# Kernel optimization log

Measured on AMD Instinct MI355X. Metric: run time of the kernel, lower is better.

The kernel has to match this reference:

```python
import jax, jax.numpy as jnp
import numpy as np

D = 192      # model dim (out_channels)
DIN = 384    # d_inner = 2*D
N = 16       # d_state
DTR = 12     # dt_rank = ceil(D/16)
K = 4        # depthwise conv kernel size
NB = 3       # total mamba blocks (2 stacked + 1 in downsample)


def setup_inputs() -> dict:
    key = jax.random.key(0)
    ks = jax.random.split(key, 8)
    rn = lambda k, shape, s: jax.random.normal(k, shape, jnp.float32) * s
    inp = {
        "x": jax.random.normal(ks[0], (2, 96, 56, 56), jnp.float32),
        "proj_w": rn(ks[1], (D, 96), 0.1),
        "proj_b": jnp.zeros((D,), jnp.float32),
        "bn_g": jnp.ones((D,), jnp.float32),
        "bn_b": jnp.zeros((D,), jnp.float32),
        "bn_mean": jnp.zeros((D,), jnp.float32),
        "bn_var": jnp.ones((D,), jnp.float32),
        "ln_g": jnp.ones((NB, D), jnp.float32),
        "ln_b": jnp.zeros((NB, D), jnp.float32),
        "Win": rn(ks[2], (NB, 2 * DIN, D), 0.05),
        "b_in": jnp.zeros((NB, 2 * DIN), jnp.float32),
        "conv_w": rn(ks[3], (NB, DIN, K), 0.2),
        "conv_b": jnp.zeros((NB, DIN), jnp.float32),
        "Wx": rn(ks[4], (NB, DTR + 2 * N, DIN), 0.05),
        "Wdt": rn(ks[5], (NB, DIN, DTR), 0.05),
        "bdt": jnp.full((NB, DIN), -4.6, jnp.float32),  # softplus ~ 0.01
        "A_log": jnp.log(jnp.broadcast_to(jnp.arange(1, N + 1, dtype=jnp.float32), (NB, DIN, N))),
        "Dskip": jnp.ones((NB, DIN), jnp.float32),
        "Wout": rn(ks[6], (NB, D, DIN), 0.05),
        "bout": jnp.zeros((NB, D), jnp.float32),
    }
    return inp


def _mamba(x, ln_g, ln_b, Win, b_in, conv_w, conv_b, Wx, Wdt, bdt, A_log, Dskip, Wout, bout):
    # x: (B, C, H, W) -> flatten spatial dims to a sequence (B, L, C)
    B, C, H, W = x.shape
    L = H * W
    seq = x.reshape(B, C, L).transpose(0, 2, 1)
    mu = seq.mean(-1, keepdims=True)
    var = seq.var(-1, keepdims=True)
    h = (seq - mu) * jax.lax.rsqrt(var + 1e-5) * ln_g + ln_b  # LayerNorm
    xz = jnp.einsum('bld,ed->ble', h, Win) + b_in              # (B, L, 2*DIN)
    xi, z = jnp.split(xz, 2, axis=-1)
    # depthwise causal conv1d along L
    xc = jnp.pad(xi.transpose(0, 2, 1), ((0, 0), (0, 0), (K - 1, 0)))
    xc = jax.lax.conv_general_dilated(xc, conv_w[:, None, :], (1,), 'VALID',
                                      feature_group_count=DIN) + conv_b[:, None]
    xi = jax.nn.silu(xc).transpose(0, 2, 1)                    # (B, L, DIN)
    proj = jnp.einsum('ble,pe->blp', xi, Wx)                   # (B, L, DTR+2N)
    dtl = proj[..., :DTR]
    Bm = proj[..., DTR:DTR + N]
    Cm = proj[..., DTR + N:]
    dt = jax.nn.softplus(jnp.einsum('blr,er->ble', dtl, Wdt) + bdt)  # (B, L, DIN)
    A = -jnp.exp(A_log)                                         # (DIN, N)
    dA = jnp.exp(dt[..., None] * A)                             # (B, L, DIN, N)
    dBx = (dt * xi)[..., None] * Bm[:, :, None, :]              # (B, L, DIN, N)

    def step(hc, t):
        dA_t, dBx_t, C_t = t
        hc = dA_t * hc + dBx_t                                  # (B, DIN, N)
        return hc, jnp.einsum('ben,bn->be', hc, C_t)

    h0 = jnp.zeros((B, DIN, N), x.dtype)
    _, ys = jax.lax.scan(step, h0, (dA.transpose(1, 0, 2, 3),
                                    dBx.transpose(1, 0, 2, 3),
                                    Cm.transpose(1, 0, 2)))
    y = ys.transpose(1, 0, 2) + Dskip * xi
    y = y * jax.nn.silu(z)
    out = jnp.einsum('ble,de->bld', y, Wout) + bout
    return out.transpose(0, 2, 1).reshape(B, C, H, W)


def _maxpool2(x):
    return jax.lax.reduce_window(x, -jnp.inf, jax.lax.max,
                                 (1, 1, 2, 2), (1, 1, 2, 2), 'VALID')


def reference(x, proj_w, proj_b, bn_g, bn_b, bn_mean, bn_var, ln_g, ln_b, Win, b_in,
              conv_w, conv_b, Wx, Wdt, bdt, A_log, Dskip, Wout, bout):
    # proj (conv1x1) + BatchNorm (eval-mode running stats)
    x = jnp.einsum('bchw,oc->bohw', x, proj_w) + proj_b[:, None, None]
    x = (x - bn_mean[:, None, None]) * jax.lax.rsqrt(bn_var[:, None, None] + 1e-5) \
        * bn_g[:, None, None] + bn_b[:, None, None]
    blk = lambda i, v: _mamba(v, ln_g[i], ln_b[i], Win[i], b_in[i], conv_w[i], conv_b[i],
                              Wx[i], Wdt[i], bdt[i], A_log[i], Dskip[i], Wout[i], bout[i])
    for i in range(2):  # residual mamba blocks
        x = x + blk(i, x)
    skip = x
    x = blk(2, _maxpool2(x))  # downsample: maxpool then mamba (no residual)
    return (x, skip)
```

## Files before the change

kernel.cpp:

```cpp
#include <hip/hip_runtime.h>

typedef __attribute__((ext_vector_type(8))) __bf16 bf16x8;
typedef __attribute__((ext_vector_type(4))) __bf16 bf16x4;
typedef __attribute__((ext_vector_type(4))) float f32x4;

#define DEV static __device__ __forceinline__

DEV float fast_rcp(float x) { return __builtin_amdgcn_rcpf(x); }
DEV float sigm(float x) { return fast_rcp(1.f + __expf(-x)); }
DEV float siluf(float x) { return x * sigm(x); }
DEV float softplusf(float x) { return x > 20.f ? x : __logf(1.f + __expf(x)); }

__global__ __launch_bounds__(256) void k_wcvt(
    const float* __restrict__ Win, const float* __restrict__ Wout,
    const float* __restrict__ Wx, __bf16* __restrict__ Wb)
{
  const int idx = blockIdx.x * 256 + threadIdx.x;
  if (idx < 442368) Wb[idx] = (__bf16)Win[idx];
  else if (idx < 663552) Wb[idx] = (__bf16)Wout[idx - 442368];
  else if (idx < 714240) Wb[idx] = (__bf16)Wx[idx - 663552];
}

__global__ __launch_bounds__(256) void k_proj(
    const float* __restrict__ x, const float* __restrict__ pw,
    const float* __restrict__ pb, const float* __restrict__ bng,
    const float* __restrict__ bnb, const float* __restrict__ bnm,
    const float* __restrict__ bnv, float* __restrict__ v)
{
  constexpr int SAP = 104;
  __shared__ __bf16 As[64 * SAP];
  __shared__ __bf16 Ws[64 * SAP];
  const int tid = threadIdx.x;
  const int r0 = blockIdx.x * 64;
  const int col0 = blockIdx.y * 64;
  const int b = r0 / 3136, l0 = r0 % 3136;
  const int lane = tid & 63, wv = tid >> 6;
  const int rh = wv >> 1, ch = wv & 1;
  const int lm = lane & 15, quad = lane >> 4;

#pragma unroll
  for (int it = 0; it < 6; ++it) {
    const int idx = tid + it * 256;
    const int c = idx >> 4, l4 = idx & 15;
    const float4 t = *(const float4*)(x + ((size_t)(b * 96 + c)) * 3136 + l0 + l4 * 4);
    As[(l4 * 4 + 0) * SAP + c] = (__bf16)t.x;
    As[(l4 * 4 + 1) * SAP + c] = (__bf16)t.y;
    As[(l4 * 4 + 2) * SAP + c] = (__bf16)t.z;
    As[(l4 * 4 + 3) * SAP + c] = (__bf16)t.w;
  }
#pragma unroll
  for (int it = 0; it < 6; ++it) {
    const int idx = tid + it * 256;
    const int wr = idx / 24, kc = (idx % 24) * 4;
    const float4 t = *(const float4*)(pw + (size_t)(col0 + wr) * 96 + kc);
    bf16x4 o;
    o[0] = (__bf16)t.x; o[1] = (__bf16)t.y; o[2] = (__bf16)t.z; o[3] = (__bf16)t.w;
    *(bf16x4*)(&Ws[wr * SAP + kc]) = o;
  }
  __syncthreads();

  f32x4 acc[2][2] = {};
#pragma unroll
  for (int ks = 0; ks < 3; ++ks) {
    const int kb = ks * 32 + quad * 8;
    bf16x8 a0 = *(const bf16x8*)(&As[(rh * 32 + lm) * SAP + kb]);
    bf16x8 a1 = *(const bf16x8*)(&As[(rh * 32 + 16 + lm) * SAP + kb]);
    bf16x8 b0 = *(const bf16x8*)(&Ws[(ch * 32 + lm) * SAP + kb]);
    bf16x8 b1 = *(const bf16x8*)(&Ws[(ch * 32 + 16 + lm) * SAP + kb]);
    acc[0][0] = __builtin_amdgcn_mfma_f32_16x16x32_bf16(a0, b0, acc[0][0], 0, 0, 0);
    acc[0][1] = __builtin_amdgcn_mfma_f32_16x16x32_bf16(a0, b1, acc[0][1], 0, 0, 0);
    acc[1][0] = __builtin_amdgcn_mfma_f32_16x16x32_bf16(a1, b0, acc[1][0], 0, 0, 0);
    acc[1][1] = __builtin_amdgcn_mfma_f32_16x16x32_bf16(a1, b1, acc[1][1], 0, 0, 0);
  }

#pragma unroll
  for (int ti = 0; ti < 2; ++ti)
#pragma unroll
    for (int tj = 0; tj < 2; ++tj) {
      const int gcol = col0 + ch * 32 + tj * 16 + lm;
      const float s = rsqrtf(bnv[gcol] + 1e-5f) * bng[gcol];
      const float sh = (pb[gcol] - bnm[gcol]) * s + bnb[gcol];
#pragma unroll
      for (int j = 0; j < 4; ++j) {
        const int grow = r0 + rh * 32 + ti * 16 + quad * 4 + j;
        v[(size_t)grow * 192 + gcol] = acc[ti][tj][j] * s + sh;
      }
    }
}

__global__ __launch_bounds__(256) void k_pool(const float* __restrict__ v, float* __restrict__ vp)
{
  const int idx = blockIdx.x * 256 + threadIdx.x;
  if (idx >= 1568 * 192) return;
  const int d = idx % 192;
  const int r2 = idx / 192;
  const int b = r2 / 784, l2 = r2 % 784;
  const int h2 = l2 / 28, w2 = l2 % 28;
  const float* p = v + (size_t)(b * 3136 + h2 * 112 + w2 * 2) * 192 + d;
  vp[idx] = fmaxf(fmaxf(p[0], p[192]), fmaxf(p[56 * 192], p[57 * 192]));
}

__global__ __launch_bounds__(256) void k_conv(
    const float* __restrict__ xz, float* __restrict__ xi, __bf16* __restrict__ xiB,
    const float* __restrict__ cw, const float* __restrict__ cb,
    int Lseq, int nthreads)
{
  const int idx = blockIdx.x * 256 + threadIdx.x;
  if (idx >= nthreads) return;
  const int e = idx % 384;
  const int seg = idx / 384;
  const int nseg = Lseq / 8;
  const int b = seg / nseg;
  const int l0 = (seg % nseg) * 8;
  const float4 w4 = *(const float4*)(cw + e * 4);
  const float bv = cb[e];
  float xv[11];
#pragma unroll
  for (int k = 0; k < 11; ++k) {
    const int l = l0 - 3 + k;
    xv[k] = (l >= 0) ? xz[(size_t)(b * Lseq + l) * 768 + e] : 0.f;
  }
#pragma unroll
  for (int j = 0; j < 8; ++j) {
    const float a = bv + xv[j] * w4.x + xv[j + 1] * w4.y + xv[j + 2] * w4.z + xv[j + 3] * w4.w;
    const float r = siluf(a);
    const size_t o = (size_t)(b * Lseq + l0 + j) * 384 + e;
    xi[o] = r;
    xiB[o] = (__bf16)r;
  }
}

constexpr int EPI_XZ = 0, EPI_G2 = 1, EPI_RES = 2, EPI_RES_SKIP = 3, EPI_OUT2 = 4;

template <int AMODE, int NT, int EPI>
__global__ __launch_bounds__(256) void k_gemm(
    const void* __restrict__ Ain, const __bf16* __restrict__ W,
    const float* __restrict__ bias, float* __restrict__ O,
    int M, int K, int Nvalid,
    float* __restrict__ dtlbuf, float* __restrict__ bcbuf,
    float* __restrict__ oflt,
    const float* __restrict__ lng, const float* __restrict__ lnb,
    int Lseq)
{
  constexpr int SA = 200;
  constexpr int CT = (NT == 1) ? 2 : 4;
  __shared__ __bf16 As[64 * SA];
  __shared__ __bf16 Ws[64 * NT * SA];
  __shared__ float lnS[(AMODE == 2) ? 384 : 1];
  const int tid = threadIdx.x;
  const int r0 = blockIdx.x * 64;
  const int col0 = blockIdx.y * (64 * NT);
  const int lane = tid & 63, wv = tid >> 6;
  const int rh = (NT == 1) ? (wv >> 1) : (wv & 1);
  const int ch = (NT == 1) ? (wv & 1) : (wv >> 1);
  const int lm = lane & 15, quad = lane >> 4;

  if constexpr (AMODE == 2) {
    if (tid < 192) { lnS[tid] = lng[tid]; lnS[192 + tid] = lnb[tid]; }
    __syncthreads();
  }

  f32x4 acc[2][CT] = {};
  const int nkp = K / 192;
  for (int kp = 0; kp < nkp; ++kp) {
    if (kp) __syncthreads();
    if constexpr (AMODE == 1) {
      const __bf16* Ab = (const __bf16*)Ain;
#pragma unroll
      for (int it = 0; it < 6; ++it) {
        const int idx = tid + it * 256;
        const int row = idx / 24, kc = (idx % 24) * 8;
        const int gr = min(r0 + row, M - 1);
        bf16x8 val = *(const bf16x8*)(Ab + (size_t)gr * K + kp * 192 + kc);
        *(bf16x8*)(&As[row * SA + kc]) = val;
      }
    } else {
      const float* A = (const float*)Ain;
      const int row = tid >> 2, part = tid & 3;
      const int gr = min(r0 + row, M - 1);
      const int cbase = part * 48;
      float4 tv[12];
#pragma unroll
      for (int j = 0; j < 12; ++j)
        tv[j] = *(const float4*)(A + (size_t)gr * 192 + cbase + j * 4);
      float s = 0.f, sq = 0.f;
#pragma unroll
      for (int j = 0; j < 12; ++j) {
        s += tv[j].x + tv[j].y + tv[j].z + tv[j].w;
        sq += tv[j].x * tv[j].x + tv[j].y * tv[j].y + tv[j].z * tv[j].z + tv[j].w * tv[j].w;
      }
      s += __shfl_xor(s, 1); s += __shfl_xor(s, 2);
      sq += __shfl_xor(sq, 1); sq += __shfl_xor(sq, 2);
      const float mean = s * (1.f / 192.f);
      const float rstd = rsqrtf(sq * (1.f / 192.f) - mean * mean + 1e-5f);
#pragma unroll
      for (int j = 0; j < 12; ++j) {
        const int c = cbase + j * 4;
        bf16x4 o;
        o[0] = (__bf16)((tv[j].x - mean) * rstd * lnS[c + 0] + lnS[192 + c + 0]);
        o[1] = (__bf16)((tv[j].y - mean) * rstd * lnS[c + 1] + lnS[192 + c + 1]);
        o[2] = (__bf16)((tv[j].z - mean) * rstd * lnS[c + 2] + lnS[192 + c + 2]);
        o[3] = (__bf16)((tv[j].w - mean) * rstd * lnS[c + 3] + lnS[192 + c + 3]);
        *(bf16x4*)(&As[row * SA + c]) = o;
      }
    }
#pragma unroll
    for (int it = 0; it < 6 * NT; ++it) {
      const int idx = tid + it * 256;
      const int wr = idx / 24, kc = (idx % 24) * 8;
      const int gw = col0 + wr;
      bf16x8 val = {};
      if (gw < Nvalid) val = *(const bf16x8*)(W + (size_t)gw * K + kp * 192 + kc);
      *(bf16x8*)(&Ws[wr * SA + kc]) = val;
    }
    __syncthreads();
#pragma unroll
    for (int ks = 0; ks < 6; ++ks) {
      const int kb = ks * 32 + quad * 8;
      bf16x8 a0 = *(const bf16x8*)(&As[(rh * 32 + lm) * SA + kb]);
      bf16x8 a1 = *(const bf16x8*)(&As[(rh * 32 + 16 + lm) * SA + kb]);
#pragma unroll
      for (int tj = 0; tj < CT; ++tj) {
        bf16x8 bfr = *(const bf16x8*)(&Ws[(ch * (16 * CT) + tj * 16 + lm) * SA + kb]);
        acc[0][tj] = __builtin_amdgcn_mfma_f32_16x16x32_bf16(a0, bfr, acc[0][tj], 0, 0, 0);
        acc[1][tj] = __builtin_amdgcn_mfma_f32_16x16x32_bf16(a1, bfr, acc[1][tj], 0, 0, 0);
      }
    }
  }

  if constexpr (EPI == EPI_G2) {
    __shared__ float dtlS[64 * 12];
#pragma unroll
    for (int ti = 0; ti < 2; ++ti)
#pragma unroll
      for (int tj = 0; tj < CT; ++tj) {
        const int colt = ch * (16 * CT) + tj * 16 + lm;
#pragma unroll
        for (int j = 0; j < 4; ++j) {
          const int rowt = rh * 32 + ti * 16 + quad * 4 + j;
          const int grow = r0 + rowt;
          const float val = acc[ti][tj][j];
          if (colt < 12) dtlS[rowt * 12 + colt] = val;
          else if (colt < 44 && grow < M)
            bcbuf[(size_t)grow * 32 + (colt - 12)] = val;
        }
      }
    __syncthreads();
    for (int idx = tid; idx < 64 * 12; idx += 256) {
      const int grow = r0 + idx / 12;
      if (grow < M) dtlbuf[(size_t)grow * 12 + idx % 12] = dtlS[idx];
    }
  } else {
#pragma unroll
    for (int ti = 0; ti < 2; ++ti)
#pragma unroll
      for (int tj = 0; tj < CT; ++tj) {
        const int colt = ch * (16 * CT) + tj * 16 + lm;
        const int gcol = col0 + colt;
        const float bv = bias[gcol];
#pragma unroll
        for (int j = 0; j < 4; ++j) {
          const int rowt = rh * 32 + ti * 16 + quad * 4 + j;
          const int grow = r0 + rowt;
          if (grow >= M) continue;
          const float val = acc[ti][tj][j] + bv;
          if constexpr (EPI == EPI_XZ) {
            O[(size_t)grow * 768 + gcol] = val;
          } else if constexpr (EPI == EPI_RES) {
            O[(size_t)grow * 192 + gcol] += val;
          } else if constexpr (EPI == EPI_RES_SKIP) {
            const float nv = O[(size_t)grow * 192 + gcol] + val;
            O[(size_t)grow * 192 + gcol] = nv;
            const int b = grow / 3136, l = grow % 3136;
            oflt[b * 602112 + gcol * 3136 + l] = nv;
          } else {
            const int b = grow / 784, l = grow % 784;
            oflt[b * 150528 + gcol * 784 + l] = val;
          }
        }
      }
  }
}

constexpr int SC_LC = 28, SC_T = 7, SC_TN = 4;

DEV void compute_dts(const float* __restrict__ dtl, const float* __restrict__ Wdt,
                     const float* __restrict__ bdt, int rowbase, int e, int t,
                     float* dtlS, float* wdtS, float* dts)
{
  for (int idx = t; idx < SC_LC * 12; idx += 128)
    dtlS[idx] = dtl[(size_t)(rowbase + idx / 12) * 12 + idx % 12];
#pragma unroll
  for (int r = 0; r < 12; ++r) wdtS[r * 128 + t] = Wdt[(size_t)e * 12 + r];
}

__global__ __launch_bounds__(128) void k_scan1(
    const float* __restrict__ dtl, const float* __restrict__ xi,
    const float* __restrict__ bc, const float* __restrict__ Wdt,
    const float* __restrict__ bdt, const float* __restrict__ A_log,
    float* __restrict__ P, float* __restrict__ S, int Lseq, int NC)
{
  __shared__ float Bs[SC_LC * 16];
  __shared__ float dts[SC_LC * 128];
  __shared__ float dtlS[SC_LC * 12];
  __shared__ float wdtS[12 * 128];
  const int t = threadIdx.x;
  const int e = blockIdx.y * 128 + t;
  const int c = blockIdx.x % NC;
  const int b = blockIdx.x / NC;
  const int rowbase = b * Lseq + c * SC_LC;

  for (int idx = t; idx < SC_LC * 16; idx += 128) {
    const int l = idx >> 4, q = idx & 15;
    Bs[idx] = bc[(size_t)(rowbase + l) * 32 + q];
  }
  compute_dts(dtl, Wdt, bdt, rowbase, e, t, dtlS, wdtS, dts);
  const float bdte = bdt[e];

  float An2[16];
  {
    const float4* a4 = (const float4*)(A_log + e * 16);
    float4 t0 = a4[0], t1 = a4[1], t2 = a4[2], t3 = a4[3];
    float tmp[16] = {t0.x, t0.y, t0.z, t0.w, t1.x, t1.y, t1.z, t1.w,
                     t2.x, t2.y, t2.z, t2.w, t3.x, t3.y, t3.z, t3.w};
#pragma unroll
    for (int n = 0; n < 16; ++n) An2[n] = -__expf(tmp[n]) * 1.44269504f;
  }
  __syncthreads();
  for (int l = 0; l < SC_LC; ++l) {
    float a = bdte;
#pragma unroll
    for (int r = 0; r < 12; ++r) a += dtlS[l * 12 + r] * wdtS[r * 128 + t];
    dts[l * 128 + t] = softplusf(a);
  }

  float h[16], ap[16];
#pragma unroll
  for (int n = 0; n < 16; ++n) { h[n] = 0.f; ap[n] = 1.f; }

  float xA[SC_T], xB[SC_T];
  auto LOADA = [&](int tt) {
#pragma unroll
    for (int j = 0; j < SC_T; ++j)
      xA[j] = xi[(size_t)(rowbase + tt * SC_T + j) * 384 + e];
  };
  auto LOADB = [&](int tt) {
#pragma unroll
    for (int j = 0; j < SC_T; ++j)
      xB[j] = xi[(size_t)(rowbase + tt * SC_T + j) * 384 + e];
  };
  auto COMP = [&](const float (&x8)[SC_T], int tt) {
#pragma unroll
    for (int j = 0; j < SC_T; ++j) {
      const int l = tt * SC_T + j;
      const float dtv = dts[l * 128 + t];
      const float u = dtv * x8[j];
      const float* Brow = &Bs[l * 16];
#pragma unroll
      for (int n = 0; n < 16; ++n) {
        const float a = __builtin_amdgcn_exp2f(dtv * An2[n]);
        h[n] = a * h[n] + u * Brow[n];
        ap[n] *= a;
      }
    }
  };

  LOADA(0);
#pragma unroll
  for (int tt = 0; tt < SC_TN; ++tt) {
    if (tt & 1) { if (tt + 1 < SC_TN) LOADA(tt + 1); COMP(xB, tt); }
    else        { if (tt + 1 < SC_TN) LOADB(tt + 1); COMP(xA, tt); }
  }

  const size_t o = ((size_t)(b * NC + c) * 384 + e) * 16;
#pragma unroll
  for (int q = 0; q < 4; ++q) {
    *(float4*)(P + o + q * 4) = make_float4(ap[q*4], ap[q*4+1], ap[q*4+2], ap[q*4+3]);
    *(float4*)(S + o + q * 4) = make_float4(h[q*4], h[q*4+1], h[q*4+2], h[q*4+3]);
  }
}

__global__ __launch_bounds__(256) void k_carry(
    const float* __restrict__ P, float* __restrict__ SH, int NC)
{
  const int tid = blockIdx.x * 256 + threadIdx.x;
  const int b = tid / 6144, r = tid % 6144;
  size_t o = (size_t)b * NC * 6144 + r;
  float h = 0.f;
  for (int c0 = 0; c0 < NC; c0 += 4) {
    float p[4], s[4];
#pragma unroll
    for (int k = 0; k < 4; ++k) { p[k] = P[o + (size_t)k * 6144]; s[k] = SH[o + (size_t)k * 6144]; }
#pragma unroll
    for (int k = 0; k < 4; ++k) { SH[o + (size_t)k * 6144] = h; h = p[k] * h + s[k]; }
    o += (size_t)4 * 6144;
  }
}

__global__ __launch_bounds__(128) void k_scan2(
    const float* __restrict__ dtl, const float* __restrict__ xi,
    const float* __restrict__ bc, const float* __restrict__ xz,
    const float* __restrict__ Wdt, const float* __restrict__ bdt,
    const float* __restrict__ A_log, const float* __restrict__ Dskip,
    const float* __restrict__ H0, __bf16* __restrict__ y, int Lseq, int NC)
{
  __shared__ float BCs[SC_LC * 32];
  __shared__ float dts[SC_LC * 128];
  __shared__ float dtlS[SC_LC * 12];
  __shared__ float wdtS[12 * 128];
  const int t = threadIdx.x;
  const int e = blockIdx.y * 128 + t;
  const int c = blockIdx.x % NC;
  const int b = blockIdx.x / NC;
  const int rowbase = b * Lseq + c * SC_LC;

  for (int idx = t; idx < SC_LC * 32; idx += 128)
    BCs[idx] = bc[(size_t)rowbase * 32 + idx];
  compute_dts(dtl, Wdt, bdt, rowbase, e, t, dtlS, wdtS, dts);
  const float bdte = bdt[e];

  float An2[16];
  {
    const float4* a4 = (const float4*)(A_log + e * 16);
    float4 t0 = a4[0], t1 = a4[1], t2 = a4[2], t3 = a4[3];
    float tmp[16] = {t0.x, t0.y, t0.z, t0.w, t1.x, t1.y, t1.z, t1.w,
                     t2.x, t2.y, t2.z, t2.w, t3.x, t3.y, t3.z, t3.w};
#pragma unroll
    for (int n = 0; n < 16; ++n) An2[n] = -__expf(tmp[n]) * 1.44269504f;
  }
  float h[16];
  {
    const size_t o = ((size_t)(b * NC + c) * 384 + e) * 16;
    const float4* h4 = (const float4*)(H0 + o);
    float4 t0 = h4[0], t1 = h4[1], t2 = h4[2], t3 = h4[3];
    h[0]=t0.x; h[1]=t0.y; h[2]=t0.z; h[3]=t0.w;
    h[4]=t1.x; h[5]=t1.y; h[6]=t1.z; h[7]=t1.w;
    h[8]=t2.x; h[9]=t2.y; h[10]=t2.z; h[11]=t2.w;
    h[12]=t3.x; h[13]=t3.y; h[14]=t3.z; h[15]=t3.w;
  }
  __syncthreads();
  for (int l = 0; l < SC_LC; ++l) {
    float a = bdte;
#pragma unroll
    for (int r = 0; r < 12; ++r) a += dtlS[l * 12 + r] * wdtS[r * 128 + t];
    dts[l * 128 + t] = softplusf(a);
  }
  const float Dse = Dskip[e];

  float xA[SC_T], zA[SC_T], xB[SC_T], zB[SC_T];
  auto LOADA = [&](int tt) {
#pragma unroll
    for (int j = 0; j < SC_T; ++j) {
      const size_t r = (size_t)(rowbase + tt * SC_T + j);
      xA[j] = xi[r * 384 + e];
      zA[j] = xz[r * 768 + 384 + e];
    }
  };
  auto LOADB = [&](int tt) {
#pragma unroll
    for (int j = 0; j < SC_T; ++j) {
      const size_t r = (size_t)(rowbase + tt * SC_T + j);
      xB[j] = xi[r * 384 + e];
      zB[j] = xz[r * 768 + 384 + e];
    }
  };
  auto COMP = [&](const float (&x8)[SC_T], const float (&z8)[SC_T], int tt) {
#pragma unroll
    for (int j = 0; j < SC_T; ++j) {
      const int l = tt * SC_T + j;
      const float dtv = dts[l * 128 + t];
      const float xiv = x8[j];
      const float u = dtv * xiv;
      const float* Brow = &BCs[l * 32];
      const float* Crow = Brow + 16;
      float yv = 0.f;
#pragma unroll
      for (int n = 0; n < 16; ++n) {
        const float a = __builtin_amdgcn_exp2f(dtv * An2[n]);
        h[n] = a * h[n] + u * Brow[n];
        yv += h[n] * Crow[n];
      }
      y[(size_t)(rowbase + l) * 384 + e] = (__bf16)((yv + Dse * xiv) * siluf(z8[j]));
    }
  };

  LOADA(0);
#pragma unroll
  for (int tt = 0; tt < SC_TN; ++tt) {
    if (tt & 1) { if (tt + 1 < SC_TN) LOADA(tt + 1); COMP(xB, zB, tt); }
    else        { if (tt + 1 < SC_TN) LOADB(tt + 1); COMP(xA, zA, tt); }
  }
}

extern "C" void kernel_launch(void* const* d_in, const int* in_sizes, int n_in,
                              void* d_out, int out_size, void* d_ws, size_t ws_size,
                              hipStream_t stream)
{
  const float* x    = (const float*)d_in[0];
  const float* pw   = (const float*)d_in[1];
  const float* pb   = (const float*)d_in[2];
  const float* bng  = (const float*)d_in[3];
  const float* bnb  = (const float*)d_in[4];
  const float* bnm  = (const float*)d_in[5];
  const float* bnv  = (const float*)d_in[6];
  const float* lng  = (const float*)d_in[7];
  const float* lnb  = (const float*)d_in[8];
  const float* Win  = (const float*)d_in[9];
  const float* b_in = (const float*)d_in[10];
  const float* cw   = (const float*)d_in[11];
  const float* cb   = (const float*)d_in[12];
  const float* Wx   = (const float*)d_in[13];
  const float* Wdt  = (const float*)d_in[14];
  const float* bdt  = (const float*)d_in[15];
  const float* Alog = (const float*)d_in[16];
  const float* Dsk  = (const float*)d_in[17];
  const float* Wout = (const float*)d_in[18];
  const float* bout = (const float*)d_in[19];

  float* wsf = (float*)d_ws;
  float* v    = wsf;
  float* xz   = v + 1204224;
  float* xib  = xz + 4816896;
  float* dtlb = xib + 2408448;
  float* bcb  = dtlb + 75264;
  float* Sb   = bcb + 200704;
  float* vp   = Sb + 1376256;
  __bf16* xiB = (__bf16*)(vp + 301056);
  __bf16* yB  = xiB;
  __bf16* Wb  = (__bf16*)(vp + 301056 + 1204224);

  float* out0 = (float*)d_out;
  float* out1 = out0 + 301056;
  float* Pbig = out0;
  float* Psml = xz + 2408448;

  k_wcvt<<<2790, 256, 0, stream>>>(Win, Wout, Wx, Wb);
  k_proj<<<dim3(98, 3), 256, 0, stream>>>(x, pw, pb, bng, bnb, bnm, bnv, v);

  for (int i = 0; i < 3; ++i) {
    const int big = (i < 2) ? 1 : 0;
    const int Lseq = big ? 3136 : 784;
    const int M = 2 * Lseq;
    const int NC = Lseq / SC_LC;
    const int MB = (M + 63) / 64;
    const float* lng_i = lng + i * 192;
    const float* lnb_i = lnb + i * 192;
    const float* bin_i = b_in + i * 768;
    const float* cw_i  = cw + i * 384 * 4;
    const float* cb_i  = cb + i * 384;
    const float* Wdt_i = Wdt + i * 384 * 12;
    const float* bdt_i = bdt + i * 384;
    const float* Al_i  = Alog + i * 384 * 16;
    const float* Ds_i  = Dsk + i * 384;
    const float* bo_i  = bout + i * 192;
    const __bf16* Winb_i  = Wb + i * 147456;
    const __bf16* Woutb_i = Wb + 442368 + i * 73728;
    const __bf16* Wxb_i   = Wb + 663552 + i * 16896;
    float* Pb = big ? Pbig : Psml;

    if (i == 2)
      k_pool<<<(1568 * 192 + 255) / 256, 256, 0, stream>>>(v, vp);
    const float* src = big ? v : vp;

    k_gemm<2, 2, EPI_XZ><<<dim3(MB, 6), 256, 0, stream>>>(
        src, Winb_i, bin_i, xz, M, 192, 768,
        nullptr, nullptr, nullptr,
        lng_i, lnb_i, Lseq);
    k_conv<<<(M * 384 / 8 + 255) / 256, 256, 0, stream>>>(
        xz, xib, xiB, cw_i, cb_i, Lseq, M * 384 / 8);
    k_gemm<1, 1, EPI_G2><<<dim3(MB, 1), 256, 0, stream>>>(
        xiB, Wxb_i, nullptr, nullptr, M, 384, 44,
        dtlb, bcb, nullptr,
        nullptr, nullptr, Lseq);
    k_scan1<<<dim3(2 * NC, 3), 128, 0, stream>>>(
        dtlb, xib, bcb, Wdt_i, bdt_i, Al_i, Pb, Sb, Lseq, NC);
    k_carry<<<48, 256, 0, stream>>>(Pb, Sb, NC);
    k_scan2<<<dim3(2 * NC, 3), 128, 0, stream>>>(
        dtlb, xib, bcb, xz, Wdt_i, bdt_i, Al_i, Ds_i, Sb, yB, Lseq, NC);
    if (i == 0)
      k_gemm<1, 1, EPI_RES><<<dim3(MB, 3), 256, 0, stream>>>(
          yB, Woutb_i, bo_i, v, M, 384, 192,
          nullptr, nullptr, nullptr,
          nullptr, nullptr, Lseq);
    else if (i == 1)
      k_gemm<1, 1, EPI_RES_SKIP><<<dim3(MB, 3), 256, 0, stream>>>(
          yB, Woutb_i, bo_i, v, M, 384, 192,
          nullptr, nullptr, out1,
          nullptr, nullptr, Lseq);
    else
      k_gemm<1, 1, EPI_OUT2><<<dim3(MB, 3), 256, 0, stream>>>(
          yB, Woutb_i, bo_i, v, M, 384, 192,
          nullptr, nullptr, out0,
          nullptr, nullptr, Lseq);
  }
}
```

Before: 397.4 us.

## Fuse weight conversion into proj, maxpool into GEMM, drop fp32 xi buffer

Merges the weight bf16 conversion kernel into the projection kernel's grid as extra blocks, folds the 2x2 maxpool into the LayerNorm A-load of the in-projection GEMM for the downsample block, and removes the fp32 copy of the conv output. The scans now read the bf16 xi instead. Together these cut two launches and a sizeable amount of global memory traffic. The cost is that the scan input loses precision because it is bf16, and yB now lives in its own buffer instead of aliasing xiB.

```diff
diff --git a/kernel.cpp b/kernel.cpp
--- a/kernel.cpp
+++ b/kernel.cpp
@@ -11,28 +11,30 @@
 DEV float siluf(float x) { return x * sigm(x); }
 DEV float softplusf(float x) { return x > 20.f ? x : __logf(1.f + __expf(x)); }
 
-__global__ __launch_bounds__(256) void k_wcvt(
-    const float* __restrict__ Win, const float* __restrict__ Wout,
-    const float* __restrict__ Wx, __bf16* __restrict__ Wb)
-{
-  const int idx = blockIdx.x * 256 + threadIdx.x;
-  if (idx < 442368) Wb[idx] = (__bf16)Win[idx];
-  else if (idx < 663552) Wb[idx] = (__bf16)Wout[idx - 442368];
-  else if (idx < 714240) Wb[idx] = (__bf16)Wx[idx - 663552];
-}
-
-__global__ __launch_bounds__(256) void k_proj(
+__global__ __launch_bounds__(256) void k_proj_wcvt(
     const float* __restrict__ x, const float* __restrict__ pw,
     const float* __restrict__ pb, const float* __restrict__ bng,
     const float* __restrict__ bnb, const float* __restrict__ bnm,
-    const float* __restrict__ bnv, float* __restrict__ v)
+    const float* __restrict__ bnv, float* __restrict__ v,
+    const float* __restrict__ Win, const float* __restrict__ Wout,
+    const float* __restrict__ Wx, __bf16* __restrict__ Wb)
 {
   constexpr int SAP = 104;
   __shared__ __bf16 As[64 * SAP];
   __shared__ __bf16 Ws[64 * SAP];
   const int tid = threadIdx.x;
-  const int r0 = blockIdx.x * 64;
-  const int col0 = blockIdx.y * 64;
+  const int bid = blockIdx.x;
+
+  if (bid >= 294) {
+    const int idx = (bid - 294) * 256 + tid;
+    if (idx < 442368) Wb[idx] = (__bf16)Win[idx];
+    else if (idx < 663552) Wb[idx] = (__bf16)Wout[idx - 442368];
+    else Wb[idx] = (__bf16)Wx[idx - 663552];
+    return;
+  }
+
+  const int r0 = (bid % 98) * 64;
+  const int col0 = (bid / 98) * 64;
   const int b = r0 / 3136, l0 = r0 % 3136;
   const int lane = tid & 63, wv = tid >> 6;
   const int rh = wv >> 1, ch = wv & 1;
@@ -88,20 +90,8 @@
     }
 }
 
-__global__ __launch_bounds__(256) void k_pool(const float* __restrict__ v, float* __restrict__ vp)
-{
-  const int idx = blockIdx.x * 256 + threadIdx.x;
-  if (idx >= 1568 * 192) return;
-  const int d = idx % 192;
-  const int r2 = idx / 192;
-  const int b = r2 / 784, l2 = r2 % 784;
-  const int h2 = l2 / 28, w2 = l2 % 28;
-  const float* p = v + (size_t)(b * 3136 + h2 * 112 + w2 * 2) * 192 + d;
-  vp[idx] = fmaxf(fmaxf(p[0], p[192]), fmaxf(p[56 * 192], p[57 * 192]));
-}
-
 __global__ __launch_bounds__(256) void k_conv(
-    const float* __restrict__ xz, float* __restrict__ xi, __bf16* __restrict__ xiB,
+    const float* __restrict__ xz, __bf16* __restrict__ xiB,
     const float* __restrict__ cw, const float* __restrict__ cb,
     int Lseq, int nthreads)
 {
@@ -123,10 +113,7 @@
 #pragma unroll
   for (int j = 0; j < 8; ++j) {
     const float a = bv + xv[j] * w4.x + xv[j + 1] * w4.y + xv[j + 2] * w4.z + xv[j + 3] * w4.w;
-    const float r = siluf(a);
-    const size_t o = (size_t)(b * Lseq + l0 + j) * 384 + e;
-    xi[o] = r;
-    xiB[o] = (__bf16)r;
+    xiB[(size_t)(b * Lseq + l0 + j) * 384 + e] = (__bf16)siluf(a);
   }
 }
 
@@ -146,7 +133,7 @@
   constexpr int CT = (NT == 1) ? 2 : 4;
   __shared__ __bf16 As[64 * SA];
   __shared__ __bf16 Ws[64 * NT * SA];
-  __shared__ float lnS[(AMODE == 2) ? 384 : 1];
+  __shared__ float lnS[(AMODE >= 2) ? 384 : 1];
   const int tid = threadIdx.x;
   const int r0 = blockIdx.x * 64;
   const int col0 = blockIdx.y * (64 * NT);
@@ -155,7 +142,7 @@
   const int ch = (NT == 1) ? (wv & 1) : (wv >> 1);
   const int lm = lane & 15, quad = lane >> 4;
 
-  if constexpr (AMODE == 2) {
+  if constexpr (AMODE >= 2) {
     if (tid < 192) { lnS[tid] = lng[tid]; lnS[192 + tid] = lnb[tid]; }
     __syncthreads();
   }
@@ -180,9 +167,27 @@
       const int gr = min(r0 + row, M - 1);
       const int cbase = part * 48;
       float4 tv[12];
-#pragma unroll
-      for (int j = 0; j < 12; ++j)
-        tv[j] = *(const float4*)(A + (size_t)gr * 192 + cbase + j * 4);
+      if constexpr (AMODE == 2) {
+#pragma unroll
+        for (int j = 0; j < 12; ++j)
+          tv[j] = *(const float4*)(A + (size_t)gr * 192 + cbase + j * 4);
+      } else {
+        const int bb = gr / 784, l2 = gr % 784;
+        const int h2 = l2 / 28, w2 = l2 % 28;
+        const float* p0 = A + (size_t)(bb * 3136 + h2 * 112 + w2 * 2) * 192;
+#pragma unroll
+        for (int j = 0; j < 12; ++j) {
+          const int cc = cbase + j * 4;
+          const float4 a0 = *(const float4*)(p0 + cc);
+          const float4 a1 = *(const float4*)(p0 + 192 + cc);
+          const float4 a2 = *(const float4*)(p0 + 56 * 192 + cc);
+          const float4 a3 = *(const float4*)(p0 + 57 * 192 + cc);
+          tv[j].x = fmaxf(fmaxf(a0.x, a1.x), fmaxf(a2.x, a3.x));
+          tv[j].y = fmaxf(fmaxf(a0.y, a1.y), fmaxf(a2.y, a3.y));
+          tv[j].z = fmaxf(fmaxf(a0.z, a1.z), fmaxf(a2.z, a3.z));
+          tv[j].w = fmaxf(fmaxf(a0.w, a1.w), fmaxf(a2.w, a3.w));
+        }
+      }
       float s = 0.f, sq = 0.f;
 #pragma unroll
       for (int j = 0; j < 12; ++j) {
@@ -286,7 +291,7 @@
 
 DEV void compute_dts(const float* __restrict__ dtl, const float* __restrict__ Wdt,
                      const float* __restrict__ bdt, int rowbase, int e, int t,
-                     float* dtlS, float* wdtS, float* dts)
+                     float* dtlS, float* wdtS)
 {
   for (int idx = t; idx < SC_LC * 12; idx += 128)
     dtlS[idx] = dtl[(size_t)(rowbase + idx / 12) * 12 + idx % 12];
@@ -295,7 +300,7 @@
 }
 
 __global__ __launch_bounds__(128) void k_scan1(
-    const float* __restrict__ dtl, const float* __restrict__ xi,
+    const float* __restrict__ dtl, const __bf16* __restrict__ xi,
     const float* __restrict__ bc, const float* __restrict__ Wdt,
     const float* __restrict__ bdt, const float* __restrict__ A_log,
     float* __restrict__ P, float* __restrict__ S, int Lseq, int NC)
@@ -314,7 +319,7 @@
     const int l = idx >> 4, q = idx & 15;
     Bs[idx] = bc[(size_t)(rowbase + l) * 32 + q];
   }
-  compute_dts(dtl, Wdt, bdt, rowbase, e, t, dtlS, wdtS, dts);
+  compute_dts(dtl, Wdt, bdt, rowbase, e, t, dtlS, wdtS);
   const float bdte = bdt[e];
 
   float An2[16];
@@ -342,12 +347,12 @@
   auto LOADA = [&](int tt) {
 #pragma unroll
     for (int j = 0; j < SC_T; ++j)
-      xA[j] = xi[(size_t)(rowbase + tt * SC_T + j) * 384 + e];
+      xA[j] = (float)xi[(size_t)(rowbase + tt * SC_T + j) * 384 + e];
   };
   auto LOADB = [&](int tt) {
 #pragma unroll
     for (int j = 0; j < SC_T; ++j)
-      xB[j] = xi[(size_t)(rowbase + tt * SC_T + j) * 384 + e];
+      xB[j] = (float)xi[(size_t)(rowbase + tt * SC_T + j) * 384 + e];
   };
   auto COMP = [&](const float (&x8)[SC_T], int tt) {
 #pragma unroll
@@ -398,7 +403,7 @@
 }
 
 __global__ __launch_bounds__(128) void k_scan2(
-    const float* __restrict__ dtl, const float* __restrict__ xi,
+    const float* __restrict__ dtl, const __bf16* __restrict__ xi,
     const float* __restrict__ bc, const float* __restrict__ xz,
     const float* __restrict__ Wdt, const float* __restrict__ bdt,
     const float* __restrict__ A_log, const float* __restrict__ Dskip,
@@ -416,7 +421,7 @@
 
   for (int idx = t; idx < SC_LC * 32; idx += 128)
     BCs[idx] = bc[(size_t)rowbase * 32 + idx];
-  compute_dts(dtl, Wdt, bdt, rowbase, e, t, dtlS, wdtS, dts);
+  compute_dts(dtl, Wdt, bdt, rowbase, e, t, dtlS, wdtS);
   const float bdte = bdt[e];
 
   float An2[16];
@@ -452,7 +457,7 @@
 #pragma unroll
     for (int j = 0; j < SC_T; ++j) {
       const size_t r = (size_t)(rowbase + tt * SC_T + j);
-      xA[j] = xi[r * 384 + e];
+      xA[j] = (float)xi[r * 384 + e];
       zA[j] = xz[r * 768 + 384 + e];
     }
   };
@@ -460,7 +465,7 @@
 #pragma unroll
     for (int j = 0; j < SC_T; ++j) {
       const size_t r = (size_t)(rowbase + tt * SC_T + j);
-      xB[j] = xi[r * 384 + e];
+      xB[j] = (float)xi[r * 384 + e];
       zB[j] = xz[r * 768 + 384 + e];
     }
   };
@@ -520,22 +525,20 @@
   float* wsf = (float*)d_ws;
   float* v    = wsf;
   float* xz   = v + 1204224;
-  float* xib  = xz + 4816896;
-  float* dtlb = xib + 2408448;
+  float* dtlb = xz + 4816896;
   float* bcb  = dtlb + 75264;
   float* Sb   = bcb + 200704;
-  float* vp   = Sb + 1376256;
-  __bf16* xiB = (__bf16*)(vp + 301056);
-  __bf16* yB  = xiB;
-  __bf16* Wb  = (__bf16*)(vp + 301056 + 1204224);
+  __bf16* xiB = (__bf16*)(Sb + 1376256);
+  __bf16* yB  = (__bf16*)(Sb + 1376256 + 1204224);
+  __bf16* Wb  = (__bf16*)(Sb + 1376256 + 2408448);
 
   float* out0 = (float*)d_out;
   float* out1 = out0 + 301056;
   float* Pbig = out0;
   float* Psml = xz + 2408448;
 
-  k_wcvt<<<2790, 256, 0, stream>>>(Win, Wout, Wx, Wb);
-  k_proj<<<dim3(98, 3), 256, 0, stream>>>(x, pw, pb, bng, bnb, bnm, bnv, v);
+  k_proj_wcvt<<<3084, 256, 0, stream>>>(x, pw, pb, bng, bnb, bnm, bnv, v,
+                                        Win, Wout, Wx, Wb);
 
   for (int i = 0; i < 3; ++i) {
     const int big = (i < 2) ? 1 : 0;
@@ -558,39 +561,35 @@
     const __bf16* Wxb_i   = Wb + 663552 + i * 16896;
     float* Pb = big ? Pbig : Psml;
 
-    if (i == 2)
-      k_pool<<<(1568 * 192 + 255) / 256, 256, 0, stream>>>(v, vp);
-    const float* src = big ? v : vp;
-
-    k_gemm<2, 2, EPI_XZ><<<dim3(MB, 6), 256, 0, stream>>>(
-        src, Winb_i, bin_i, xz, M, 192, 768,
-        nullptr, nullptr, nullptr,
-        lng_i, lnb_i, Lseq);
+    if (big)
+      k_gemm<2, 2, EPI_XZ><<<dim3(MB, 6), 256, 0, stream>>>(
+          v, Winb_i, bin_i, xz, M, 192, 768,
+          nullptr, nullptr, nullptr, lng_i, lnb_i, Lseq);
+    else
+      k_gemm<3, 2, EPI_XZ><<<dim3(MB, 6), 256, 0, stream>>>(
+          v, Winb_i, bin_i, xz, M, 192, 768,
+          nullptr, nullptr, nullptr, lng_i, lnb_i, Lseq);
     k_conv<<<(M * 384 / 8 + 255) / 256, 256, 0, stream>>>(
-        xz, xib, xiB, cw_i, cb_i, Lseq, M * 384 / 8);
+        xz, xiB, cw_i, cb_i, Lseq, M * 384 / 8);
     k_gemm<1, 1, EPI_G2><<<dim3(MB, 1), 256, 0, stream>>>(
         xiB, Wxb_i, nullptr, nullptr, M, 384, 44,
-        dtlb, bcb, nullptr,
-        nullptr, nullptr, Lseq);
+        dtlb, bcb, nullptr, nullptr, nullptr, Lseq);
     k_scan1<<<dim3(2 * NC, 3), 128, 0, stream>>>(
-        dtlb, xib, bcb, Wdt_i, bdt_i, Al_i, Pb, Sb, Lseq, NC);
+        dtlb, xiB, bcb, Wdt_i, bdt_i, Al_i, Pb, Sb, Lseq, NC);
     k_carry<<<48, 256, 0, stream>>>(Pb, Sb, NC);
     k_scan2<<<dim3(2 * NC, 3), 128, 0, stream>>>(
-        dtlb, xib, bcb, xz, Wdt_i, bdt_i, Al_i, Ds_i, Sb, yB, Lseq, NC);
+        dtlb, xiB, bcb, xz, Wdt_i, bdt_i, Al_i, Ds_i, Sb, yB, Lseq, NC);
     if (i == 0)
       k_gemm<1, 1, EPI_RES><<<dim3(MB, 3), 256, 0, stream>>>(
           yB, Woutb_i, bo_i, v, M, 384, 192,
-          nullptr, nullptr, nullptr,
-          nullptr, nullptr, Lseq);
+          nullptr, nullptr, nullptr, nullptr, nullptr, Lseq);
     else if (i == 1)
       k_gemm<1, 1, EPI_RES_SKIP><<<dim3(MB, 3), 256, 0, stream>>>(
           yB, Woutb_i, bo_i, v, M, 384, 192,
-          nullptr, nullptr, out1,
-          nullptr, nullptr, Lseq);
+          nullptr, nullptr, out1, nullptr, nullptr, Lseq);
     else
       k_gemm<1, 1, EPI_OUT2><<<dim3(MB, 3), 256, 0, stream>>>(
           yB, Woutb_i, bo_i, v, M, 384, 192,
-          nullptr, nullptr, out0,
-          nullptr, nullptr, Lseq);
-  }
-}
+          nullptr, nullptr, out0, nullptr, nullptr, Lseq);
+  }
+}
```

Measured after the change: 394.1 us. About the same (-0.8%).
